# Kernel optimization log

Measured on AMD Instinct MI355X. Metric: run time of the kernel, lower is better.

The kernel has to match this reference:

```python
import jax, jax.numpy as jnp
import numpy as np

N_HEAD = 8
DQK = 64
DV = 64
D_IN = 512
D_OUT = 512
D_MID = 2048
B = 4
L = 2048
EPS = 1e-5


def layernorm(x):
    mu = jnp.mean(x, axis=-1, keepdims=True)
    var = jnp.mean(jnp.square(x - mu), axis=-1, keepdims=True)
    return (x - mu) / jnp.sqrt(var + EPS)


def setup_inputs() -> dict:
    key = jax.random.key(0)
    ks = jax.random.split(key, 10)
    s = 0.02
    return {
        "query": jax.random.normal(ks[0], (B, L, D_IN), jnp.float32),
        "key": jax.random.normal(ks[1], (B, L, D_IN), jnp.float32),
        "value": jax.random.normal(ks[2], (B, L, D_IN), jnp.float32),
        "mask": jnp.zeros((B, L, L), jnp.float32),
        "WQ": jax.random.normal(ks[3], (D_IN, N_HEAD * DQK), jnp.float32) * s,
        "WK": jax.random.normal(ks[4], (D_IN, N_HEAD * DQK), jnp.float32) * s,
        "WV": jax.random.normal(ks[5], (D_IN, N_HEAD * DV), jnp.float32) * s,
        "WO": jax.random.normal(ks[6], (N_HEAD * DV, D_OUT), jnp.float32) * s,
        "W1": jax.random.normal(ks[7], (D_OUT, D_MID), jnp.float32) * s,
        "W2": jax.random.normal(ks[8], (D_MID, D_OUT), jnp.float32) * s,
    }


def reference(query, key, value, mask, WQ, WK, WV, WO, W1, W2):
    bsz = query.shape[0]
    # projections -> [b, h, l, d]
    Q = (query @ WQ).reshape(bsz, -1, N_HEAD, DQK).transpose(0, 2, 1, 3)
    K = (key @ WK).reshape(bsz, -1, N_HEAD, DQK).transpose(0, 2, 1, 3)
    V = (value @ WV).reshape(bsz, -1, N_HEAD, DV).transpose(0, 2, 1, 3)
    # scaled dot-product attention with additive mask [b, 1, lq, lk]
    scores = jnp.einsum("bhqd,bhkd->bhqk", Q, K) / jnp.sqrt(jnp.float32(DQK))
    w = jax.nn.softmax(scores + mask[:, None, :, :], axis=-1)
    out = jnp.einsum("bhqk,bhkd->bhqd", w, V)
    out = out.transpose(0, 2, 1, 3).reshape(bsz, -1, N_HEAD * DV)
    out = out @ WO
    out = layernorm(query + out)
    ff = jax.nn.relu(out @ W1) @ W2
    return layernorm(out + ff)
```

## Files before the change

### kernel.cpp

```cpp
#include <hip/hip_runtime.h>
#include <hip/hip_bf16.h>

using bf16 = __bf16;
typedef __bf16 bf16x4 __attribute__((ext_vector_type(4)));
typedef __bf16 bf16x8 __attribute__((ext_vector_type(8)));
typedef float f32x4 __attribute__((ext_vector_type(4)));

static constexpr int BATCH = 4;
static constexpr int SEQ   = 2048;
static constexpr int DIN   = 512;
static constexpr int NHEAD = 8;
static constexpr int DMID  = 2048;
static constexpr int MROWS = BATCH * SEQ;

__device__ __forceinline__ void gload16(const void* g, void* l)
{
    __builtin_amdgcn_global_load_lds(
        (const __attribute__((address_space(1))) unsigned int*)g,
        (__attribute__((address_space(3))) unsigned int*)l, 16, 0, 0);
}

__global__ __launch_bounds__(256) void mask_check(const uint4* __restrict__ m,
                                                  int* __restrict__ flag)
{
    const int base = (blockIdx.x * 256 + threadIdx.x) * 4;
    unsigned nz = 0;
    for (int i = 0; i < 4; ++i) {
        const uint4 v = m[base + i];
        nz |= v.x | v.y | v.z | v.w;
    }
    if (nz) atomicOr(flag, 1);
}

__global__ __launch_bounds__(256) void transpose_weights(
    const float* __restrict__ WQ, const float* __restrict__ WK,
    const float* __restrict__ WV, const float* __restrict__ WO,
    const float* __restrict__ W1, const float* __restrict__ W2,
    bf16* __restrict__ WQt, bf16* __restrict__ WKt, bf16* __restrict__ WVt,
    bf16* __restrict__ WOt, bf16* __restrict__ W1t, bf16* __restrict__ W2t)
{
    __shared__ float tile[32][33];
    const int bid = blockIdx.x;
    const float* in; bf16* out; int ip, op, cx, ry;
    if (bid < 1024) {
        const int w = bid >> 8, idx = bid & 255;
        in  = w == 0 ? WQ  : w == 1 ? WK  : w == 2 ? WV  : WO;
        out = w == 0 ? WQt : w == 1 ? WKt : w == 2 ? WVt : WOt;
        ip = 512; op = 512; cx = idx & 15; ry = idx >> 4;
    } else if (bid < 2048) {
        const int idx = bid - 1024;
        in = W1; out = W1t; ip = 2048; op = 512; cx = idx & 63; ry = idx >> 6;
    } else {
        const int idx = bid - 2048;
        in = W2; out = W2t; ip = 512; op = 2048; cx = idx & 15; ry = idx >> 4;
    }
    const int c0 = cx * 32, r0 = ry * 32;
    const int tx = threadIdx.x & 31, ty = threadIdx.x >> 5;
    for (int i = 0; i < 32; i += 8)
        tile[ty + i][tx] = in[(size_t)(r0 + ty + i) * ip + c0 + tx];
    __syncthreads();
    for (int i = 0; i < 32; i += 8)
        out[(size_t)(c0 + ty + i) * op + r0 + tx] = (bf16)tile[tx][ty + i];
}

__global__ __launch_bounds__(256) void transpose_b2b(const bf16* __restrict__ in,
                                                     bf16* __restrict__ out,
                                                     int ip, int op)
{
    __shared__ bf16 tile[32][33];
    const int c0 = blockIdx.x * 32;
    const int r0 = blockIdx.y * 32;
    const int tx = threadIdx.x & 31;
    const int ty = threadIdx.x >> 5;
    for (int i = 0; i < 32; i += 8)
        tile[ty + i][tx] = in[(size_t)(r0 + ty + i) * ip + c0 + tx];
    __syncthreads();
    for (int i = 0; i < 32; i += 8)
        out[(size_t)(c0 + ty + i) * op + r0 + tx] = tile[tx][ty + i];
}

template <int ACT>
__global__ __launch_bounds__(256) void gemm128(const bf16* __restrict__ A,
                                               const bf16* __restrict__ Bt,
                                               bf16* __restrict__ C,
                                               int N, int K)
{
    __shared__ bf16 sA[128 * 64];
    __shared__ bf16 sB[128 * 64];

    const int t    = threadIdx.x;
    const int lane = t & 63;
    const int wave = t >> 6;
    const int wm   = wave >> 1;
    const int wn   = wave & 1;
    const int lr   = lane & 15;
    const int lq   = lane >> 4;

    const int m0 = blockIdx.y * 128;
    const int n0 = blockIdx.x * 128;

    const int srow = lane >> 3;
    const int scol = (lane & 7) * 8;

    f32x4 acc[4][4] = {};

    for (int k0 = 0; k0 < K; k0 += 64) {
        if (k0) __syncthreads();
#pragma unroll
        for (int i = 0; i < 4; ++i) {
            const int ch = wave * 4 + i;
            const int r  = ch * 8 + srow;
            gload16(A  + (size_t)(m0 + r) * K + k0 + scol, sA + ch * 512);
            gload16(Bt + (size_t)(n0 + r) * K + k0 + scol, sB + ch * 512);
        }
        __syncthreads();

#pragma unroll
        for (int kk = 0; kk < 2; ++kk) {
            bf16x8 af[4], bfr[4];
#pragma unroll
            for (int x = 0; x < 4; ++x) {
                af[x]  = *reinterpret_cast<const bf16x8*>(&sA[(wm * 64 + x * 16 + lr) * 64 + kk * 32 + lq * 8]);
                bfr[x] = *reinterpret_cast<const bf16x8*>(&sB[(wn * 64 + x * 16 + lr) * 64 + kk * 32 + lq * 8]);
            }
#pragma unroll
            for (int m = 0; m < 4; ++m)
#pragma unroll
                for (int n = 0; n < 4; ++n)
                    acc[m][n] = __builtin_amdgcn_mfma_f32_16x16x32_bf16(af[m], bfr[n], acc[m][n], 0, 0, 0);
        }
    }

#pragma unroll
    for (int n = 0; n < 4; ++n) {
        const int col = n0 + wn * 64 + n * 16 + lr;
#pragma unroll
        for (int m = 0; m < 4; ++m) {
            const int rowb = m0 + wm * 64 + m * 16 + lq * 4;
#pragma unroll
            for (int j = 0; j < 4; ++j) {
                float v = acc[m][n][j];
                if (ACT == 1) v = v > 0.f ? v : 0.f;
                C[(size_t)(rowb + j) * N + col] = (bf16)v;
            }
        }
    }
}

template <int ACT, bool AF32>
__device__ __forceinline__ void gemm64_body(const void* __restrict__ Ain,
                                            const bf16* __restrict__ Bt,
                                            bf16* __restrict__ C,
                                            int N, int K,
                                            bf16* sA, bf16* sB)
{
    const int t    = threadIdx.x;
    const int lane = t & 63;
    const int wave = t >> 6;
    const int lr   = lane & 15;
    const int lq   = lane >> 4;

    const int m0 = blockIdx.y * 64;
    const int n0 = blockIdx.x * 128;

    const int srow = lane >> 3;
    const int scol = (lane & 7) * 8;

    f32x4 acc[4][2] = {};

    for (int k0 = 0; k0 < K; k0 += 64) {
        if constexpr (AF32) {
            const float* Af = (const float*)Ain;
            float4 fa[4];
#pragma unroll
            for (int i = 0; i < 2; ++i) {
                const float* p = Af + (size_t)(m0 + (wave * 2 + i) * 8 + srow) * K + k0 + scol;
                fa[2 * i]     = *reinterpret_cast<const float4*>(p);
                fa[2 * i + 1] = *reinterpret_cast<const float4*>(p + 4);
            }
            if (k0) __syncthreads();
#pragma unroll
            for (int i = 0; i < 4; ++i) {
                const int ch = wave * 4 + i;
                gload16(Bt + (size_t)(n0 + ch * 8 + srow) * K + k0 + scol, sB + ch * 512);
            }
#pragma unroll
            for (int i = 0; i < 2; ++i) {
                const int r = (wave * 2 + i) * 8 + srow;
                const float4 a = fa[2 * i], b = fa[2 * i + 1];
                bf16x8 hh;
                hh[0] = (bf16)a.x; hh[1] = (bf16)a.y; hh[2] = (bf16)a.z; hh[3] = (bf16)a.w;
                hh[4] = (bf16)b.x; hh[5] = (bf16)b.y; hh[6] = (bf16)b.z; hh[7] = (bf16)b.w;
                *reinterpret_cast<bf16x8*>(&sA[r * 64 + scol]) = hh;
            }
        } else {
            const bf16* Ab = (const bf16*)Ain;
            if (k0) __syncthreads();
#pragma unroll
            for (int i = 0; i < 2; ++i) {
                const int ch = wave * 2 + i;
                gload16(Ab + (size_t)(m0 + ch * 8 + srow) * K + k0 + scol, sA + ch * 512);
            }
#pragma unroll
            for (int i = 0; i < 4; ++i) {
                const int ch = wave * 4 + i;
                gload16(Bt + (size_t)(n0 + ch * 8 + srow) * K + k0 + scol, sB + ch * 512);
            }
        }
        __syncthreads();

#pragma unroll
        for (int kk = 0; kk < 2; ++kk) {
            bf16x8 af[4], bfr[2];
#pragma unroll
            for (int x = 0; x < 4; ++x)
                af[x] = *reinterpret_cast<const bf16x8*>(&sA[(x * 16 + lr) * 64 + kk * 32 + lq * 8]);
#pragma unroll
            for (int n = 0; n < 2; ++n)
                bfr[n] = *reinterpret_cast<const bf16x8*>(&sB[(wave * 32 + n * 16 + lr) * 64 + kk * 32 + lq * 8]);
#pragma unroll
            for (int m = 0; m < 4; ++m)
#pragma unroll
                for (int n = 0; n < 2; ++n)
                    acc[m][n] = __builtin_amdgcn_mfma_f32_16x16x32_bf16(af[m], bfr[n], acc[m][n], 0, 0, 0);
        }
    }

#pragma unroll
    for (int n = 0; n < 2; ++n) {
        const int col = n0 + wave * 32 + n * 16 + lr;
#pragma unroll
        for (int m = 0; m < 4; ++m) {
            const int rowb = m0 + m * 16 + lq * 4;
#pragma unroll
            for (int j = 0; j < 4; ++j) {
                float v = acc[m][n][j];
                if (ACT == 1) v = v > 0.f ? v : 0.f;
                C[(size_t)(rowb + j) * N + col] = (bf16)v;
            }
        }
    }
}

template <int ACT>
__global__ __launch_bounds__(256) void gemm64(const bf16* __restrict__ A,
                                              const bf16* __restrict__ Bt,
                                              bf16* __restrict__ C,
                                              int N, int K)
{
    __shared__ bf16 sA[64 * 64];
    __shared__ bf16 sB[128 * 64];
    gemm64_body<ACT, false>(A, Bt, C, N, K, sA, sB);
}

__global__ __launch_bounds__(256) void gemm64_qkv(const float* __restrict__ q,
                                                  const float* __restrict__ k,
                                                  const float* __restrict__ v,
                                                  const bf16* __restrict__ WQt,
                                                  const bf16* __restrict__ WKt,
                                                  const bf16* __restrict__ WVt,
                                                  bf16* __restrict__ Qb,
                                                  bf16* __restrict__ Kb,
                                                  bf16* __restrict__ Vb)
{
    __shared__ bf16 sA[64 * 64];
    __shared__ bf16 sB[128 * 64];
    const void* A  = blockIdx.z == 0 ? (const void*)q : blockIdx.z == 1 ? (const void*)k : (const void*)v;
    const bf16* Bt = blockIdx.z == 0 ? WQt : blockIdx.z == 1 ? WKt : WVt;
    bf16*       C  = blockIdx.z == 0 ? Qb  : blockIdx.z == 1 ? Kb  : Vb;
    gemm64_body<0, true>(A, Bt, C, DIN, DIN, sA, sB);
}

__global__ __launch_bounds__(256) void attn_kernel(const bf16* __restrict__ Qb,
                                                   const bf16* __restrict__ Kb,
                                                   const bf16* __restrict__ Vt,
                                                   const float* __restrict__ mask,
                                                   bf16* __restrict__ O,
                                                   const int* __restrict__ mzf)
{
    const int bi   = blockIdx.x;
    const int xcd  = bi & 7;
    const int slot = bi >> 3;
    const int pair = xcd * 4 + (slot >> 4);
    const int qt   = slot & 15;
    const int h    = pair >> 2;
    const int b    = pair & 3;

    const int t    = threadIdx.x;
    const int lane = t & 63;
    const int wave = t >> 6;
    const int lr   = lane & 15;
    const int lq   = lane >> 4;
    const int q0   = qt * 128;
    const bool useM = (*mzf != 0);

    __shared__ bf16 sK[64 * 72];
    __shared__ bf16 sV[64 * 72];
    __shared__ bf16 sP[4][32 * 72];
    __shared__ bf16 sM[128 * 68];

    bf16x8 qf[2][2];
#pragma unroll
    for (int g = 0; g < 2; ++g) {
        const int qrow = q0 + wave * 32 + g * 16 + lr;
        const bf16* qp = Qb + (size_t)(b * SEQ + qrow) * DIN + h * 64 + lq * 8;
        qf[g][0] = *reinterpret_cast<const bf16x8*>(qp);
        qf[g][1] = *reinterpret_cast<const bf16x8*>(qp + 32);
    }

    f32x4 o[2][4] = {};
    f32x4 lrow[2] = {};

    const int sr = t >> 2;
    const int sc = (t & 3) << 3;

    const bf16*  kbase = Kb + (size_t)(b * SEQ) * DIN + h * 64;
    const bf16*  vbase = Vt + (size_t)(h * 64 + sr) * MROWS + b * SEQ;
    const float* mbase = mask + ((size_t)b * SEQ + q0) * SEQ;

    constexpr float L2E = 1.4426950408889634f;
    constexpr float SCL = 0.125f * L2E;
    const bf16x8 ones = {(bf16)1.f, (bf16)1.f, (bf16)1.f, (bf16)1.f,
                         (bf16)1.f, (bf16)1.f, (bf16)1.f, (bf16)1.f};

    int4 kr0 = *reinterpret_cast<const int4*>(kbase + (size_t)sr * DIN + sc);
    int4 kr1 = *reinterpret_cast<const int4*>(kbase + (size_t)sr * DIN + sc + 32);
    int4 vr0 = *reinterpret_cast<const int4*>(vbase + sc);
    int4 vr1 = *reinterpret_cast<const int4*>(vbase + sc + 32);

    for (int tile = 0; tile < SEQ / 64; ++tile) {
        if (tile) __syncthreads();

        *reinterpret_cast<int4*>(&sK[sr * 72 + sc])      = kr0;
        *reinterpret_cast<int4*>(&sK[sr * 72 + sc + 32]) = kr1;
        *reinterpret_cast<int4*>(&sV[sr * 72 + sc])      = vr0;
        *reinterpret_cast<int4*>(&sV[sr * 72 + sc + 32]) = vr1;
        if (useM) {
            const int k0 = tile * 64;
#pragma unroll
            for (int i = 0; i < 8; ++i) {
                const int idx = t + 256 * i;
                const float4 mr = *reinterpret_cast<const float4*>(
                    mbase + (size_t)(idx >> 4) * SEQ + k0 + (idx & 15) * 4);
                bf16x4 mv;
                mv[0] = (bf16)(mr.x * L2E); mv[1] = (bf16)(mr.y * L2E);
                mv[2] = (bf16)(mr.z * L2E); mv[3] = (bf16)(mr.w * L2E);
                *reinterpret_cast<bf16x4*>(&sM[(idx >> 4) * 68 + (idx & 15) * 4]) = mv;
            }
        }

        if (tile + 1 < SEQ / 64) {
            const int k0 = (tile + 1) * 64;
            kr0 = *reinterpret_cast<const int4*>(kbase + (size_t)(k0 + sr) * DIN + sc);
            kr1 = *reinterpret_cast<const int4*>(kbase + (size_t)(k0 + sr) * DIN + sc + 32);
            vr0 = *reinterpret_cast<const int4*>(vbase + k0 + sc);
            vr1 = *reinterpret_cast<const int4*>(vbase + k0 + sc + 32);
        }
        __syncthreads();

        bf16x8 kf[2][4];
#pragma unroll
        for (int s = 0; s < 2; ++s)
#pragma unroll
            for (int ni = 0; ni < 4; ++ni)
                kf[s][ni] = *reinterpret_cast<const bf16x8*>(&sK[(ni * 16 + lr) * 72 + s * 32 + lq * 8]);

#pragma unroll
        for (int g = 0; g < 2; ++g) {
            f32x4 sf[4] = {};
#pragma unroll
            for (int s = 0; s < 2; ++s)
#pragma unroll
                for (int ni = 0; ni < 4; ++ni)
                    sf[ni] = __builtin_amdgcn_mfma_f32_16x16x32_bf16(qf[g][s], kf[s][ni], sf[ni], 0, 0, 0);

            if (useM) {
#pragma unroll
                for (int j = 0; j < 4; ++j) {
                    const int mr2 = (wave * 32 + g * 16 + lq * 4 + j) * 68;
#pragma unroll
                    for (int ni = 0; ni < 4; ++ni) {
                        const float mval = (float)sM[mr2 + ni * 16 + lr];
                        sP[wave][(g * 16 + lq * 4 + j) * 72 + ni * 16 + lr] = (bf16)exp2f(sf[ni][j] * SCL + mval);
                    }
                }
            } else {
#pragma unroll
                for (int j = 0; j < 4; ++j)
#pragma unroll
                    for (int ni = 0; ni < 4; ++ni)
                        sP[wave][(g * 16 + lq * 4 + j) * 72 + ni * 16 + lr] = (bf16)exp2f(sf[ni][j] * SCL);
            }
        }

        bf16x8 vf[2][4];
#pragma unroll
        for (int s = 0; s < 2; ++s)
#pragma unroll
            for (int ni = 0; ni < 4; ++ni)
                vf[s][ni] = *reinterpret_cast<const bf16x8*>(&sV[(ni * 16 + lr) * 72 + s * 32 + lq * 8]);

#pragma unroll
        for (int g = 0; g < 2; ++g) {
            f32x4 rs = {};
#pragma unroll
            for (int s = 0; s < 2; ++s) {
                bf16x8 pf = *reinterpret_cast<const bf16x8*>(&sP[wave][(g * 16 + lr) * 72 + s * 32 + lq * 8]);
                rs = __builtin_amdgcn_mfma_f32_16x16x32_bf16(pf, ones, rs, 0, 0, 0);
#pragma unroll
                for (int ni = 0; ni < 4; ++ni)
                    o[g][ni] = __builtin_amdgcn_mfma_f32_16x16x32_bf16(pf, vf[s][ni], o[g][ni], 0, 0, 0);
            }
#pragma unroll
            for (int j = 0; j < 4; ++j)
                lrow[g][j] += rs[j];
        }
    }

#pragma unroll
    for (int g = 0; g < 2; ++g)
#pragma unroll
        for (int ni = 0; ni < 4; ++ni)
#pragma unroll
            for (int j = 0; j < 4; ++j) {
                const int row = q0 + wave * 32 + g * 16 + lq * 4 + j;
                const int col = h * 64 + ni * 16 + lr;
                O[(size_t)(b * SEQ + row) * DIN + col] = (bf16)(o[g][ni][j] / lrow[g][j]);
            }
}

__global__ __launch_bounds__(256) void add_ln(const float* __restrict__ X,
                                              const bf16* __restrict__ Y,
                                              bf16* __restrict__ Ob,
                                              float* __restrict__ Of)
{
    const int row  = blockIdx.x * 4 + (threadIdx.x >> 6);
    const int lane = threadIdx.x & 63;
    const size_t base = (size_t)row * DIN + lane * 8;
    const float4 x0 = *reinterpret_cast<const float4*>(X + base);
    const float4 x1 = *reinterpret_cast<const float4*>(X + base + 4);
    const bf16x8 yv = *reinterpret_cast<const bf16x8*>(Y + base);
    float v[8] = {x0.x, x0.y, x0.z, x0.w, x1.x, x1.y, x1.z, x1.w};
    float s = 0.f;
    for (int i = 0; i < 8; ++i) { v[i] += (float)yv[i]; s += v[i]; }
    for (int off = 1; off < 64; off <<= 1) s += __shfl_xor(s, off);
    const float mu = s * (1.f / DIN);
    float var = 0.f;
    for (int i = 0; i < 8; ++i) { const float d = v[i] - mu; var += d * d; }
    for (int off = 1; off < 64; off <<= 1) var += __shfl_xor(var, off);
    const float rstd = rsqrtf(var * (1.f / DIN) + 1e-5f);
    float r[8];
    for (int i = 0; i < 8; ++i) r[i] = (v[i] - mu) * rstd;
    if (Ob) {
        bf16x8 ov;
        for (int i = 0; i < 8; ++i) ov[i] = (bf16)r[i];
        *reinterpret_cast<bf16x8*>(Ob + base) = ov;
    }
    if (Of) {
        *reinterpret_cast<float4*>(Of + base)     = make_float4(r[0], r[1], r[2], r[3]);
        *reinterpret_cast<float4*>(Of + base + 4) = make_float4(r[4], r[5], r[6], r[7]);
    }
}

extern "C" void kernel_launch(void* const* d_in, const int* in_sizes, int n_in,
                              void* d_out, int out_size, void* d_ws, size_t ws_size,
                              hipStream_t stream)
{
    const float* query = (const float*)d_in[0];
    const float* key   = (const float*)d_in[1];
    const float* value = (const float*)d_in[2];
    const float* mask  = (const float*)d_in[3];
    const float* WQ    = (const float*)d_in[4];
    const float* WK    = (const float*)d_in[5];
    const float* WV    = (const float*)d_in[6];
    const float* WO    = (const float*)d_in[7];
    const float* W1    = (const float*)d_in[8];
    const float* W2    = (const float*)d_in[9];

    char* w = (char*)d_ws;
    size_t off = 0;
    auto carve2 = [&](size_t elems) { bf16* p = (bf16*)(w + off); off += elems * 2; return p; };
    auto carve4 = [&](size_t elems) { float* p = (float*)(w + off); off += elems * 4; return p; };

    bf16* Qb    = carve2((size_t)MROWS * DIN);
    bf16* Kb    = carve2((size_t)MROWS * DIN);
    bf16* Vb    = carve2((size_t)MROWS * DIN);
    bf16* Vt    = carve2((size_t)MROWS * DIN);
    bf16* Mid   = carve2((size_t)MROWS * DMID);
    float* Ln1f = carve4((size_t)MROWS * DIN);
    bf16* WQt   = carve2((size_t)DIN * DIN);
    bf16* WKt   = carve2((size_t)DIN * DIN);
    bf16* WVt   = carve2((size_t)DIN * DIN);
    bf16* WOt   = carve2((size_t)DIN * DIN);
    bf16* W1t   = carve2((size_t)DIN * DMID);
    bf16* W2t   = carve2((size_t)DMID * DIN);
    int*  mzf   = (int*)(w + off); off += 16;
    if (off > ws_size) return;

    bf16* Ob   = Vb;
    bf16* Two  = Qb;
    bf16* Ln1b = Kb;
    bf16* F2   = Vt;

    const dim3 blk(256);

    hipMemsetAsync(mzf, 0, 4, stream);
    mask_check<<<dim3(4096), blk, 0, stream>>>((const uint4*)mask, mzf);

    transpose_weights<<<dim3(3072), blk, 0, stream>>>(WQ, WK, WV, WO, W1, W2,
                                                      WQt, WKt, WVt, WOt, W1t, W2t);

    gemm64_qkv<<<dim3(DIN / 128, MROWS / 64, 3), blk, 0, stream>>>(query, key, value,
                                                                   WQt, WKt, WVt, Qb, Kb, Vb);

    transpose_b2b<<<dim3(DIN / 32, MROWS / 32), blk, 0, stream>>>(Vb, Vt, DIN, MROWS);

    attn_kernel<<<dim3(512), blk, 0, stream>>>(Qb, Kb, Vt, mask, Ob, mzf);

    gemm64<0><<<dim3(DIN / 128, MROWS / 64), blk, 0, stream>>>(Ob, WOt, Two, DIN, DIN);
    add_ln<<<dim3(MROWS / 4), blk, 0, stream>>>(query, Two, Ln1b, Ln1f);

    gemm128<1><<<dim3(DMID / 128, MROWS / 128), blk, 0, stream>>>(Ln1b, W1t, Mid, DMID, DIN);
    gemm64<0><<<dim3(DIN / 128, MROWS / 64), blk, 0, stream>>>(Mid, W2t, F2, DIN, DMID);

    add_ln<<<dim3(MROWS / 4), blk, 0, stream>>>(Ln1f, F2, (bf16*)nullptr, (float*)d_out);
}
```

Baseline: 367.6 us.

## Fuse residual layernorm into output GEMMs, V transpose into QKV, mask check into weight prep

Replaces the WO and W2 GEMMs plus their add+layernorm kernels with a full-row GEMM (32 rows x 512 cols per block, 512 threads, double-buffered LDS) that adds the residual and normalizes in the epilogue. The V projection now writes transposed output through LDS directly, which removes the separate transpose kernel. The mask-zero check is merged into the weight-transpose launch. These cut launches and intermediate global round trips. In exchange the fused GEMM uses about 132KB of LDS and only 256 blocks, which may limit occupancy and parallelism.

After: 370.4 us. No clear change (+0.8%).

```diff
diff --git a/kernel.cpp b/kernel.cpp
--- a/kernel.cpp
+++ b/kernel.cpp
@@ -20,27 +20,27 @@
         (__attribute__((address_space(3))) unsigned int*)l, 16, 0, 0);
 }
 
-__global__ __launch_bounds__(256) void mask_check(const uint4* __restrict__ m,
-                                                  int* __restrict__ flag)
-{
-    const int base = (blockIdx.x * 256 + threadIdx.x) * 4;
-    unsigned nz = 0;
-    for (int i = 0; i < 4; ++i) {
-        const uint4 v = m[base + i];
-        nz |= v.x | v.y | v.z | v.w;
-    }
-    if (nz) atomicOr(flag, 1);
-}
-
-__global__ __launch_bounds__(256) void transpose_weights(
+__global__ __launch_bounds__(256) void tw_mask(
     const float* __restrict__ WQ, const float* __restrict__ WK,
     const float* __restrict__ WV, const float* __restrict__ WO,
     const float* __restrict__ W1, const float* __restrict__ W2,
     bf16* __restrict__ WQt, bf16* __restrict__ WKt, bf16* __restrict__ WVt,
-    bf16* __restrict__ WOt, bf16* __restrict__ W1t, bf16* __restrict__ W2t)
-{
+    bf16* __restrict__ WOt, bf16* __restrict__ W1t, bf16* __restrict__ W2t,
+    const uint4* __restrict__ mask, int* __restrict__ flag)
+{
+    const int bid = blockIdx.x;
+    if (bid >= 3072) {
+        const uint4* p = mask + (size_t)(bid - 3072) * 4096;
+        unsigned nz = 0;
+#pragma unroll
+        for (int i = 0; i < 16; ++i) {
+            const uint4 v = p[i * 256 + threadIdx.x];
+            nz |= v.x | v.y | v.z | v.w;
+        }
+        if (nz) atomicOr(flag, 1);
+        return;
+    }
     __shared__ float tile[32][33];
-    const int bid = blockIdx.x;
     const float* in; bf16* out; int ip, op, cx, ry;
     if (bid < 1024) {
         const int w = bid >> 8, idx = bid & 255;
@@ -63,22 +63,6 @@
         out[(size_t)(c0 + ty + i) * op + r0 + tx] = (bf16)tile[tx][ty + i];
 }
 
-__global__ __launch_bounds__(256) void transpose_b2b(const bf16* __restrict__ in,
-                                                     bf16* __restrict__ out,
-                                                     int ip, int op)
-{
-    __shared__ bf16 tile[32][33];
-    const int c0 = blockIdx.x * 32;
-    const int r0 = blockIdx.y * 32;
-    const int tx = threadIdx.x & 31;
-    const int ty = threadIdx.x >> 5;
-    for (int i = 0; i < 32; i += 8)
-        tile[ty + i][tx] = in[(size_t)(r0 + ty + i) * ip + c0 + tx];
-    __syncthreads();
-    for (int i = 0; i < 32; i += 8)
-        out[(size_t)(c0 + ty + i) * op + r0 + tx] = tile[tx][ty + i];
-}
-
 template <int ACT>
 __global__ __launch_bounds__(256) void gemm128(const bf16* __restrict__ A,
                                                const bf16* __restrict__ Bt,
@@ -145,112 +129,6 @@
             }
         }
     }
-}
-
-template <int ACT, bool AF32>
-__device__ __forceinline__ void gemm64_body(const void* __restrict__ Ain,
-                                            const bf16* __restrict__ Bt,
-                                            bf16* __restrict__ C,
-                                            int N, int K,
-                                            bf16* sA, bf16* sB)
-{
-    const int t    = threadIdx.x;
-    const int lane = t & 63;
-    const int wave = t >> 6;
-    const int lr   = lane & 15;
-    const int lq   = lane >> 4;
-
-    const int m0 = blockIdx.y * 64;
-    const int n0 = blockIdx.x * 128;
-
-    const int srow = lane >> 3;
-    const int scol = (lane & 7) * 8;
-
-    f32x4 acc[4][2] = {};
-
-    for (int k0 = 0; k0 < K; k0 += 64) {
-        if constexpr (AF32) {
-            const float* Af = (const float*)Ain;
-            float4 fa[4];
-#pragma unroll
-            for (int i = 0; i < 2; ++i) {
-                const float* p = Af + (size_t)(m0 + (wave * 2 + i) * 8 + srow) * K + k0 + scol;
-                fa[2 * i]     = *reinterpret_cast<const float4*>(p);
-                fa[2 * i + 1] = *reinterpret_cast<const float4*>(p + 4);
-            }
-            if (k0) __syncthreads();
-#pragma unroll
-            for (int i = 0; i < 4; ++i) {
-                const int ch = wave * 4 + i;
-                gload16(Bt + (size_t)(n0 + ch * 8 + srow) * K + k0 + scol, sB + ch * 512);
-            }
-#pragma unroll
-            for (int i = 0; i < 2; ++i) {
-                const int r = (wave * 2 + i) * 8 + srow;
-                const float4 a = fa[2 * i], b = fa[2 * i + 1];
-                bf16x8 hh;
-                hh[0] = (bf16)a.x; hh[1] = (bf16)a.y; hh[2] = (bf16)a.z; hh[3] = (bf16)a.w;
-                hh[4] = (bf16)b.x; hh[5] = (bf16)b.y; hh[6] = (bf16)b.z; hh[7] = (bf16)b.w;
-                *reinterpret_cast<bf16x8*>(&sA[r * 64 + scol]) = hh;
-            }
-        } else {
-            const bf16* Ab = (const bf16*)Ain;
-            if (k0) __syncthreads();
-#pragma unroll
-            for (int i = 0; i < 2; ++i) {
-                const int ch = wave * 2 + i;
-                gload16(Ab + (size_t)(m0 + ch * 8 + srow) * K + k0 + scol, sA + ch * 512);
-            }
-#pragma unroll
-            for (int i = 0; i < 4; ++i) {
-                const int ch = wave * 4 + i;
-                gload16(Bt + (size_t)(n0 + ch * 8 + srow) * K + k0 + scol, sB + ch * 512);
-            }
-        }
-        __syncthreads();
-
-#pragma unroll
-        for (int kk = 0; kk < 2; ++kk) {
-            bf16x8 af[4], bfr[2];
-#pragma unroll
-            for (int x = 0; x < 4; ++x)
-                af[x] = *reinterpret_cast<const bf16x8*>(&sA[(x * 16 + lr) * 64 + kk * 32 + lq * 8]);
-#pragma unroll
-            for (int n = 0; n < 2; ++n)
-                bfr[n] = *reinterpret_cast<const bf16x8*>(&sB[(wave * 32 + n * 16 + lr) * 64 + kk * 32 + lq * 8]);
-#pragma unroll
-            for (int m = 0; m < 4; ++m)
-#pragma unroll
-                for (int n = 0; n < 2; ++n)
-                    acc[m][n] = __builtin_amdgcn_mfma_f32_16x16x32_bf16(af[m], bfr[n], acc[m][n], 0, 0, 0);
-        }
-    }
-
-#pragma unroll
-    for (int n = 0; n < 2; ++n) {
-        const int col = n0 + wave * 32 + n * 16 + lr;
-#pragma unroll
-        for (int m = 0; m < 4; ++m) {
-            const int rowb = m0 + m * 16 + lq * 4;
-#pragma unroll
-            for (int j = 0; j < 4; ++j) {
-                float v = acc[m][n][j];
-                if (ACT == 1) v = v > 0.f ? v : 0.f;
-                C[(size_t)(rowb + j) * N + col] = (bf16)v;
-            }
-        }
-    }
-}
-
-template <int ACT>
-__global__ __launch_bounds__(256) void gemm64(const bf16* __restrict__ A,
-                                              const bf16* __restrict__ Bt,
-                                              bf16* __restrict__ C,
-                                              int N, int K)
-{
-    __shared__ bf16 sA[64 * 64];
-    __shared__ bf16 sB[128 * 64];
-    gemm64_body<ACT, false>(A, Bt, C, N, K, sA, sB);
 }
 
 __global__ __launch_bounds__(256) void gemm64_qkv(const float* __restrict__ q,
@@ -261,14 +139,101 @@
                                                   const bf16* __restrict__ WVt,
                                                   bf16* __restrict__ Qb,
                                                   bf16* __restrict__ Kb,
-                                                  bf16* __restrict__ Vb)
+                                                  bf16* __restrict__ Vt)
 {
     __shared__ bf16 sA[64 * 64];
     __shared__ bf16 sB[128 * 64];
-    const void* A  = blockIdx.z == 0 ? (const void*)q : blockIdx.z == 1 ? (const void*)k : (const void*)v;
-    const bf16* Bt = blockIdx.z == 0 ? WQt : blockIdx.z == 1 ? WKt : WVt;
-    bf16*       C  = blockIdx.z == 0 ? Qb  : blockIdx.z == 1 ? Kb  : Vb;
-    gemm64_body<0, true>(A, Bt, C, DIN, DIN, sA, sB);
+
+    const float* A  = blockIdx.z == 0 ? q   : blockIdx.z == 1 ? k   : v;
+    const bf16*  Bt = blockIdx.z == 0 ? WQt : blockIdx.z == 1 ? WKt : WVt;
+    const int K = DIN;
+
+    const int t    = threadIdx.x;
+    const int lane = t & 63;
+    const int wave = t >> 6;
+    const int lr   = lane & 15;
+    const int lq   = lane >> 4;
+
+    const int m0 = blockIdx.y * 64;
+    const int n0 = blockIdx.x * 128;
+
+    const int srow = lane >> 3;
+    const int scol = (lane & 7) * 8;
+
+    f32x4 acc[4][2] = {};
+
+    for (int k0 = 0; k0 < K; k0 += 64) {
+        float4 fa[4];
+#pragma unroll
+        for (int i = 0; i < 2; ++i) {
+            const float* p = A + (size_t)(m0 + (wave * 2 + i) * 8 + srow) * K + k0 + scol;
+            fa[2 * i]     = *reinterpret_cast<const float4*>(p);
+            fa[2 * i + 1] = *reinterpret_cast<const float4*>(p + 4);
+        }
+        if (k0) __syncthreads();
+#pragma unroll
+        for (int i = 0; i < 4; ++i) {
+            const int ch = wave * 4 + i;
+            gload16(Bt + (size_t)(n0 + ch * 8 + srow) * K + k0 + scol, sB + ch * 512);
+        }
+#pragma unroll
+        for (int i = 0; i < 2; ++i) {
+            const int r = (wave * 2 + i) * 8 + srow;
+            const float4 a = fa[2 * i], b = fa[2 * i + 1];
+            bf16x8 hh;
+            hh[0] = (bf16)a.x; hh[1] = (bf16)a.y; hh[2] = (bf16)a.z; hh[3] = (bf16)a.w;
+            hh[4] = (bf16)b.x; hh[5] = (bf16)b.y; hh[6] = (bf16)b.z; hh[7] = (bf16)b.w;
+            *reinterpret_cast<bf16x8*>(&sA[r * 64 + scol]) = hh;
+        }
+        __syncthreads();
+
+#pragma unroll
+        for (int kk = 0; kk < 2; ++kk) {
+            bf16x8 af[4], bfr[2];
+#pragma unroll
+            for (int x = 0; x < 4; ++x)
+                af[x] = *reinterpret_cast<const bf16x8*>(&sA[(x * 16 + lr) * 64 + kk * 32 + lq * 8]);
+#pragma unroll
+            for (int n = 0; n < 2; ++n)
+                bfr[n] = *reinterpret_cast<const bf16x8*>(&sB[(wave * 32 + n * 16 + lr) * 64 + kk * 32 + lq * 8]);
+#pragma unroll
+            for (int m = 0; m < 4; ++m)
+#pragma unroll
+                for (int n = 0; n < 2; ++n)
+                    acc[m][n] = __builtin_amdgcn_mfma_f32_16x16x32_bf16(af[m], bfr[n], acc[m][n], 0, 0, 0);
+        }
+    }
+
+    if (blockIdx.z < 2) {
+        bf16* C = blockIdx.z == 0 ? Qb : Kb;
+#pragma unroll
+        for (int n = 0; n < 2; ++n) {
+            const int col = n0 + wave * 32 + n * 16 + lr;
+#pragma unroll
+            for (int m = 0; m < 4; ++m) {
+                const int rowb = m0 + m * 16 + lq * 4;
+#pragma unroll
+                for (int j = 0; j < 4; ++j)
+                    C[(size_t)(rowb + j) * DIN + col] = (bf16)acc[m][n][j];
+            }
+        }
+    } else {
+        __syncthreads();
+#pragma unroll
+        for (int n = 0; n < 2; ++n)
+#pragma unroll
+            for (int m = 0; m < 4; ++m)
+#pragma unroll
+                for (int j = 0; j < 4; ++j)
+                    sB[(wave * 32 + n * 16 + lr) * 64 + m * 16 + lq * 4 + j] = (bf16)acc[m][n][j];
+        __syncthreads();
+        const int c = t >> 1, half = t & 1;
+#pragma unroll
+        for (int qq = 0; qq < 4; ++qq) {
+            const bf16x8 vv = *reinterpret_cast<const bf16x8*>(&sB[c * 64 + half * 32 + qq * 8]);
+            *reinterpret_cast<bf16x8*>(Vt + (size_t)(n0 + c) * MROWS + m0 + half * 32 + qq * 8) = vv;
+        }
+    }
 }
 
 __global__ __launch_bounds__(256) void attn_kernel(const bf16* __restrict__ Qb,
@@ -429,37 +394,133 @@
             }
 }
 
-__global__ __launch_bounds__(256) void add_ln(const float* __restrict__ X,
-                                              const bf16* __restrict__ Y,
-                                              bf16* __restrict__ Ob,
-                                              float* __restrict__ Of)
-{
-    const int row  = blockIdx.x * 4 + (threadIdx.x >> 6);
-    const int lane = threadIdx.x & 63;
-    const size_t base = (size_t)row * DIN + lane * 8;
-    const float4 x0 = *reinterpret_cast<const float4*>(X + base);
-    const float4 x1 = *reinterpret_cast<const float4*>(X + base + 4);
-    const bf16x8 yv = *reinterpret_cast<const bf16x8*>(Y + base);
-    float v[8] = {x0.x, x0.y, x0.z, x0.w, x1.x, x1.y, x1.z, x1.w};
-    float s = 0.f;
-    for (int i = 0; i < 8; ++i) { v[i] += (float)yv[i]; s += v[i]; }
-    for (int off = 1; off < 64; off <<= 1) s += __shfl_xor(s, off);
-    const float mu = s * (1.f / DIN);
-    float var = 0.f;
-    for (int i = 0; i < 8; ++i) { const float d = v[i] - mu; var += d * d; }
-    for (int off = 1; off < 64; off <<= 1) var += __shfl_xor(var, off);
-    const float rstd = rsqrtf(var * (1.f / DIN) + 1e-5f);
-    float r[8];
-    for (int i = 0; i < 8; ++i) r[i] = (v[i] - mu) * rstd;
-    if (Ob) {
-        bf16x8 ov;
-        for (int i = 0; i < 8; ++i) ov[i] = (bf16)r[i];
-        *reinterpret_cast<bf16x8*>(Ob + base) = ov;
-    }
-    if (Of) {
-        *reinterpret_cast<float4*>(Of + base)     = make_float4(r[0], r[1], r[2], r[3]);
-        *reinterpret_cast<float4*>(Of + base + 4) = make_float4(r[4], r[5], r[6], r[7]);
-    }
+__global__ __launch_bounds__(512) void gemm_ln(const bf16* __restrict__ A,
+                                               const bf16* __restrict__ Bt,
+                                               const float* __restrict__ X,
+                                               bf16* __restrict__ Onb,
+                                               float* __restrict__ Onf,
+                                               int K)
+{
+    __shared__ bf16 sA[2][32 * 64];
+    __shared__ bf16 sB[2][512 * 64];
+    __shared__ float sRed[32][8];
+    __shared__ float sMu[32];
+    __shared__ float sRstd[32];
+
+    const int t    = threadIdx.x;
+    const int lane = t & 63;
+    const int w    = t >> 6;
+    const int lr   = lane & 15;
+    const int lq   = lane >> 4;
+    const int srow = lane >> 3;
+    const int scol = (lane & 7) * 8;
+
+    const int m0 = blockIdx.x * 32;
+
+    auto stage = [&](int s, int b) {
+        const int k0 = s * 64;
+#pragma unroll
+        for (int i = 0; i < 8; ++i) {
+            const int ch = w * 8 + i;
+            gload16(Bt + (size_t)(ch * 8 + srow) * K + k0 + scol, &sB[b][ch * 512]);
+        }
+        if (w < 4)
+            gload16(A + (size_t)(m0 + w * 8 + srow) * K + k0 + scol, &sA[b][w * 512]);
+    };
+
+    f32x4 acc[2][4] = {};
+    const int steps = K / 64;
+
+    stage(0, 0);
+    __syncthreads();
+
+    for (int s = 0; s < steps; ++s) {
+        const int b = s & 1;
+        if (s + 1 < steps) stage(s + 1, b ^ 1);
+
+#pragma unroll
+        for (int kk = 0; kk < 2; ++kk) {
+            bf16x8 af[2], bfr[4];
+#pragma unroll
+            for (int m = 0; m < 2; ++m)
+                af[m] = *reinterpret_cast<const bf16x8*>(&sA[b][(m * 16 + lr) * 64 + kk * 32 + lq * 8]);
+#pragma unroll
+            for (int n = 0; n < 4; ++n)
+                bfr[n] = *reinterpret_cast<const bf16x8*>(&sB[b][(w * 64 + n * 16 + lr) * 64 + kk * 32 + lq * 8]);
+#pragma unroll
+            for (int m = 0; m < 2; ++m)
+#pragma unroll
+                for (int n = 0; n < 4; ++n)
+                    acc[m][n] = __builtin_amdgcn_mfma_f32_16x16x32_bf16(af[m], bfr[n], acc[m][n], 0, 0, 0);
+        }
+        __syncthreads();
+    }
+
+#pragma unroll
+    for (int m = 0; m < 2; ++m)
+#pragma unroll
+        for (int n = 0; n < 4; ++n)
+#pragma unroll
+            for (int j = 0; j < 4; ++j)
+                acc[m][n][j] += X[(size_t)(m0 + m * 16 + lq * 4 + j) * DIN + w * 64 + n * 16 + lr];
+
+#pragma unroll
+    for (int m = 0; m < 2; ++m)
+#pragma unroll
+        for (int j = 0; j < 4; ++j) {
+            float s = acc[m][0][j] + acc[m][1][j] + acc[m][2][j] + acc[m][3][j];
+            s += __shfl_xor(s, 1); s += __shfl_xor(s, 2);
+            s += __shfl_xor(s, 4); s += __shfl_xor(s, 8);
+            if (lr == 0) sRed[m * 16 + lq * 4 + j][w] = s;
+        }
+    __syncthreads();
+    if (t < 32) {
+        float s = 0.f;
+#pragma unroll
+        for (int ww = 0; ww < 8; ++ww) s += sRed[t][ww];
+        sMu[t] = s * (1.f / DIN);
+    }
+    __syncthreads();
+
+#pragma unroll
+    for (int m = 0; m < 2; ++m)
+#pragma unroll
+        for (int j = 0; j < 4; ++j) {
+            const float mu = sMu[m * 16 + lq * 4 + j];
+            float s = 0.f;
+#pragma unroll
+            for (int n = 0; n < 4; ++n) {
+                const float d = acc[m][n][j] - mu;
+                s += d * d;
+            }
+            s += __shfl_xor(s, 1); s += __shfl_xor(s, 2);
+            s += __shfl_xor(s, 4); s += __shfl_xor(s, 8);
+            if (lr == 0) sRed[m * 16 + lq * 4 + j][w] = s;
+        }
+    __syncthreads();
+    if (t < 32) {
+        float s = 0.f;
+#pragma unroll
+        for (int ww = 0; ww < 8; ++ww) s += sRed[t][ww];
+        sRstd[t] = rsqrtf(s * (1.f / DIN) + 1e-5f);
+    }
+    __syncthreads();
+
+#pragma unroll
+    for (int m = 0; m < 2; ++m)
+#pragma unroll
+        for (int j = 0; j < 4; ++j) {
+            const int rl = m * 16 + lq * 4 + j;
+            const float mu = sMu[rl], rstd = sRstd[rl];
+            const size_t rowoff = (size_t)(m0 + rl) * DIN;
+#pragma unroll
+            for (int n = 0; n < 4; ++n) {
+                const float r = (acc[m][n][j] - mu) * rstd;
+                const int col = w * 64 + n * 16 + lr;
+                if (Onb) Onb[rowoff + col] = (bf16)r;
+                if (Onf) Onf[rowoff + col] = r;
+            }
+        }
 }
 
 extern "C" void kernel_launch(void* const* d_in, const int* in_sizes, int n_in,
@@ -498,30 +559,25 @@
     if (off > ws_size) return;
 
     bf16* Ob   = Vb;
-    bf16* Two  = Qb;
     bf16* Ln1b = Kb;
-    bf16* F2   = Vt;
 
     const dim3 blk(256);
 
     hipMemsetAsync(mzf, 0, 4, stream);
-    mask_check<<<dim3(4096), blk, 0, stream>>>((const uint4*)mask, mzf);
-
-    transpose_weights<<<dim3(3072), blk, 0, stream>>>(WQ, WK, WV, WO, W1, W2,
-                                                      WQt, WKt, WVt, WOt, W1t, W2t);
+
+    tw_mask<<<dim3(4096), blk, 0, stream>>>(WQ, WK, WV, WO, W1, W2,
+                                            WQt, WKt, WVt, WOt, W1t, W2t,
+                                            (const uint4*)mask, mzf);
 
     gemm64_qkv<<<dim3(DIN / 128, MROWS / 64, 3), blk, 0, stream>>>(query, key, value,
-                                                                   WQt, WKt, WVt, Qb, Kb, Vb);
-
-    transpose_b2b<<<dim3(DIN / 32, MROWS / 32), blk, 0, stream>>>(Vb, Vt, DIN, MROWS);
+                                                                   WQt, WKt, WVt, Qb, Kb, Vt);
 
     attn_kernel<<<dim3(512), blk, 0, stream>>>(Qb, Kb, Vt, mask, Ob, mzf);
 
-    gemm64<0><<<dim3(DIN / 128, MROWS / 64), blk, 0, stream>>>(Ob, WOt, Two, DIN, DIN);
-    add_ln<<<dim3(MROWS / 4), blk, 0, stream>>>(query, Two, Ln1b, Ln1f);
+    gemm_ln<<<dim3(MROWS / 32), dim3(512), 0, stream>>>(Ob, WOt, query, Ln1b, Ln1f, DIN);
 
     gemm128<1><<<dim3(DMID / 128, MROWS / 128), blk, 0, stream>>>(Ln1b, W1t, Mid, DMID, DIN);
-    gemm64<0><<<dim3(DIN / 128, MROWS / 64), blk, 0, stream>>>(Mid, W2t, F2, DIN, DMID);
-
-    add_ln<<<dim3(MROWS / 4), blk, 0, stream>>>(Ln1f, F2, (bf16*)nullptr, (float*)d_out);
-}
+
+    gemm_ln<<<dim3(MROWS / 32), dim3(512), 0, stream>>>(Mid, W2t, Ln1f,
+                                                        (bf16*)nullptr, (float*)d_out, DMID);
+}
```
